# Kernel tuning notes

Hardware: AMD Instinct MI355X
Metric: run time of the kernel (lower is better)

Reference implementation:

```python
import jax, jax.numpy as jnp
import numpy as np

L, I, H = 4, 256, 512          # layers, input_size, hidden_size
SH, LH, GH = 4, 2, 2            # short/long/global heads
NH, HD, FF = SH + LH + GH, H // (SH + LH + GH), 2 * H
S, B = 1024, 8                  # seq (AST nodes), batch
EPS = 1e-5
NEG = -1e9


def _ln(x, g, b):
    m = jnp.mean(x, axis=-1, keepdims=True)
    v = jnp.var(x, axis=-1, keepdims=True)
    return (x - m) * jax.lax.rsqrt(v + EPS) * g + b


def setup_inputs() -> dict:
    key = jax.random.key(0)
    ks = jax.random.split(key, 10)
    w = lambda k, shape: jax.random.normal(k, shape, jnp.float32) * 0.02
    return {
        "nodes": jax.random.normal(ks[0], (S, B, I), jnp.float32),
        "dist": jax.random.randint(ks[1], (B, S, S), 0, 5, jnp.int32),
        "dense_w": w(ks[2], (H, I)), "dense_b": jnp.zeros((H,), jnp.float32),
        "dense_ln_g": jnp.ones((H,), jnp.float32), "dense_ln_b": jnp.zeros((H,), jnp.float32),
        "qkv_w": w(ks[3], (L, 3 * H, H)), "qkv_b": jnp.zeros((L, 3 * H), jnp.float32),
        "out_w": w(ks[4], (L, H, H)), "out_b": jnp.zeros((L, H), jnp.float32),
        "ln1_g": jnp.ones((L, H), jnp.float32), "ln1_b": jnp.zeros((L, H), jnp.float32),
        "ffn_w1": w(ks[5], (L, FF, H)), "ffn_b1": jnp.zeros((L, FF), jnp.float32),
        "ffn_w2": w(ks[6], (L, H, FF)), "ffn_b2": jnp.zeros((L, H), jnp.float32),
        "ln2_g": jnp.ones((L, H), jnp.float32), "ln2_b": jnp.zeros((L, H), jnp.float32),
        "bn_g": jnp.ones((H,), jnp.float32), "bn_b": jnp.zeros((H,), jnp.float32),
    }


def _mask_bias(dist):
    # dist: [B,S,S] int -> additive bias [B,NH,S,S]
    short = (dist == 1)[:, None]                       # [B,1,S,S]
    longm = (dist >= 1)[:, None]
    globm = jnp.broadcast_to((dist[:, 0:1, :] >= 1)[:, None], (dist.shape[0], 1, S, S))
    allowed = jnp.concatenate([
        jnp.broadcast_to(short, (dist.shape[0], SH, S, S)),
        jnp.broadcast_to(longm, (dist.shape[0], LH, S, S)),
        jnp.broadcast_to(globm, (dist.shape[0], GH, S, S)),
    ], axis=1)
    allowed = allowed | jnp.eye(S, dtype=bool)
    return jnp.where(allowed, 0.0, NEG).astype(jnp.float32)


def _forward(nodes, dist, dense_w, dense_b, dense_ln_g, dense_ln_b,
             qkv_w, qkv_b, out_w, out_b, ln1_g, ln1_b,
             ffn_w1, ffn_b1, ffn_w2, ffn_b2, ln2_g, ln2_b, bn_g, bn_b):
    x = jnp.transpose(nodes, (1, 0, 2))                # [B,S,I]
    x = _ln(x @ dense_w.T + dense_b, dense_ln_g, dense_ln_b)  # [B,S,H]
    bias = _mask_bias(dist)                            # [B,NH,S,S]
    scale = 1.0 / np.sqrt(HD)

    def layer(x, p):
        (wqkv, bqkv, wo, bo, g1, b1, w1, bf1, w2, bf2, g2, b2) = p
        qkv = x @ wqkv.T + bqkv                        # [B,S,3H]
        q, k, v = jnp.split(qkv, 3, axis=-1)
        q = q.reshape(B, S, NH, HD).transpose(0, 2, 1, 3)
        k = k.reshape(B, S, NH, HD).transpose(0, 2, 1, 3)
        v = v.reshape(B, S, NH, HD).transpose(0, 2, 1, 3)
        scores = jnp.einsum('bhqd,bhkd->bhqk', q, k) * scale + bias
        attn = jax.nn.softmax(scores, axis=-1)
        o = jnp.einsum('bhqk,bhkd->bhqd', attn, v)
        o = o.transpose(0, 2, 1, 3).reshape(B, S, H) @ wo.T + bo
        x = _ln(x + o, g1, b1)
        f = jax.nn.relu(x @ w1.T + bf1) @ w2.T + bf2
        x = _ln(x + f, g2, b2)
        return x, None

    params = (qkv_w, qkv_b, out_w, out_b, ln1_g, ln1_b,
              ffn_w1, ffn_b1, ffn_w2, ffn_b2, ln2_g, ln2_b)
    x, _ = jax.lax.scan(layer, x, params)
    hidden = x[:, 0]                                   # first token -> [B,H]
    m = jnp.mean(hidden, axis=0)
    v = jnp.var(hidden, axis=0)
    return (hidden - m) * jax.lax.rsqrt(v + EPS) * bn_g + bn_b


def reference(nodes, dist, dense_w, dense_b, dense_ln_g, dense_ln_b,
              qkv_w, qkv_b, out_w, out_b, ln1_g, ln1_b,
              ffn_w1, ffn_b1, ffn_w2, ffn_b2, ln2_g, ln2_b, bn_g, bn_b):
    return _forward(nodes, dist, dense_w, dense_b, dense_ln_g, dense_ln_b,
                    qkv_w, qkv_b, out_w, out_b, ln1_g, ln1_b,
                    ffn_w1, ffn_b1, ffn_w2, ffn_b2, ln2_g, ln2_b, bn_g, bn_b)
```

## Files before the change

### kernel.cpp

```cpp
#include <hip/hip_runtime.h>
#include <hip/hip_bf16.h>
#include <math.h>

#define LAYERS 4
#define IDIM 256
#define HDIM 512
#define NH 8
#define HD 64
#define FF 1024
#define SEQ 1024
#define BATCH 8
#define EPS 1e-5f

typedef __attribute__((ext_vector_type(8))) short short8;
typedef __attribute__((ext_vector_type(4))) short short4v;
typedef __attribute__((ext_vector_type(4))) float f32x4;
typedef __attribute__((ext_vector_type(4))) int int4v;
typedef __attribute__((ext_vector_type(4))) unsigned int uint4v;
typedef unsigned long long u64;

__device__ __forceinline__ short f2bf(float f) {
    unsigned u = __float_as_uint(f);
    u = (u + 0x7FFFu + ((u >> 16) & 1u)) >> 16;
    return (short)u;
}
__device__ __forceinline__ float bf2f(short s) {
    return __uint_as_float(((unsigned)(unsigned short)s) << 16);
}
__device__ __forceinline__ void gll16(const void* g, void* l) {
    __builtin_amdgcn_global_load_lds(
        (const __attribute__((address_space(1))) unsigned int*)g,
        (__attribute__((address_space(3))) unsigned int*)l, 16, 0, 0);
}
__device__ __forceinline__ float fexp2(float x) {
#if __has_builtin(__builtin_amdgcn_exp2f)
    return __builtin_amdgcn_exp2f(x);
#else
    return exp2f(x);
#endif
}

#define CVT_P0 131072u
#define CVT_P1 3276800u
#define CVT_P2 4325376u
#define CVT_P3 6422528u
#define CVT_TOT 8519680u
#define PREP_W 8320
#define PREP_N 2048
__global__ __launch_bounds__(256) void prep_all(
    const float* __restrict__ s0, short* __restrict__ d0,
    const float* __restrict__ s1, short* __restrict__ d1,
    const float* __restrict__ s2, short* __restrict__ d2,
    const float* __restrict__ s3, short* __restrict__ d3,
    const float* __restrict__ s4, short* __restrict__ d4,
    const float* __restrict__ nodes, short* __restrict__ xt,
    const int* __restrict__ dist, u64* __restrict__ mS,
    u64* __restrict__ mL, u64* __restrict__ mG) {
    int blk = blockIdx.x;
    if (blk < PREP_W) {
        size_t i = ((size_t)blk * 256 + threadIdx.x) * 4;
        const float* s; short* d; size_t off;
        if (i < CVT_P0)      { s = s0; d = d0; off = i; }
        else if (i < CVT_P1) { s = s1; d = d1; off = i - CVT_P0; }
        else if (i < CVT_P2) { s = s2; d = d2; off = i - CVT_P1; }
        else if (i < CVT_P3) { s = s3; d = d3; off = i - CVT_P2; }
        else                 { s = s4; d = d4; off = i - CVT_P3; }
        f32x4 f = *(const f32x4*)(s + off);
        short4v o = {f2bf(f[0]), f2bf(f[1]), f2bf(f[2]), f2bf(f[3])};
        *(short4v*)(d + off) = o;
    } else if (blk < PREP_W + PREP_N) {
        size_t idx = ((size_t)(blk - PREP_W) * 256 + threadIdx.x) * 4;
        int i  = idx & (IDIM - 1);
        int sb = idx >> 8;
        int b  = sb & (BATCH - 1);
        int s  = sb >> 3;
        f32x4 f = *(const f32x4*)(nodes + idx);
        short4v o = {f2bf(f[0]), f2bf(f[1]), f2bf(f[2]), f2bf(f[3])};
        *(short4v*)(xt + ((size_t)b * SEQ + s) * IDIM + i) = o;
    } else {
        int blk2 = blk - (PREP_W + PREP_N);
        int b = blk2 >> 10, q = blk2 & 1023;
        int wv = threadIdx.x >> 6, lane = threadIdx.x & 63;
        const int* dp = dist + ((size_t)b * SEQ + q) * SEQ;
        size_t mbase = ((size_t)b * SEQ + q) * 16;
#pragma unroll
        for (int it = 0; it < 4; it++) {
            int w64 = it * 4 + wv;
            int d = dp[w64 * 64 + lane];
            u64 bs = __ballot(d == 1);
            u64 bl = __ballot(d >= 1);
            if (lane == 0) {
                mS[mbase + w64] = bs;
                mL[mbase + w64] = bl;
                if (q == 0) mG[b * 16 + w64] = bl;
            }
        }
    }
}

template<int BM, int BK>
__global__ __launch_bounds__(256, 2)
void gemm_bf16(const short* __restrict__ A, const short* __restrict__ W,
               const float* __restrict__ bias, short* __restrict__ C,
               short* __restrict__ vt, int M, int N, int K, int relu) {
    constexpr int UPR = BK / 8;
    constexpr int RPC = 512 / BK;
    __shared__ __align__(16) short As[BM * BK];
    __shared__ __align__(16) short Ws[128 * BK];
    const int tid = threadIdx.x;
    const int w = tid >> 6, lane = tid & 63;
    const int l15 = lane & 15, quad = lane >> 4;
    const int m0 = blockIdx.y * BM, n0 = blockIdx.x * 128;

    constexpr int NI = (BM == 128) ? 4 : 2;
    const int wm = (BM == 128) ? (w >> 1) * 64 : 0;
    const int wn = (BM == 128) ? (w & 1) * 64 : w * 32;

    f32x4 acc[4][NI];
#pragma unroll
    for (int mi = 0; mi < 4; mi++)
#pragma unroll
        for (int ni = 0; ni < NI; ni++) acc[mi][ni] = (f32x4){0.f, 0.f, 0.f, 0.f};

    const int r_in = (BK == 64) ? (lane >> 3) : (lane >> 4);
    const int c8   = lane & (UPR - 1);

    for (int k0 = 0; k0 < K; k0 += BK) {
#pragma unroll
        for (int rep = 0; rep < BM * BK / 2048; rep++) {
            int chunk = rep * 4 + w;
            int row = chunk * RPC + r_in;
            const short* src = A + (size_t)(m0 + row) * K + k0 + ((c8 ^ (row & (UPR - 1))) << 3);
            gll16(src, (char*)As + chunk * 1024);
        }
#pragma unroll
        for (int rep = 0; rep < 128 * BK / 2048; rep++) {
            int chunk = rep * 4 + w;
            int row = chunk * RPC + r_in;
            const short* src = W + (size_t)(n0 + row) * K + k0 + ((c8 ^ (row & (UPR - 1))) << 3);
            gll16(src, (char*)Ws + chunk * 1024);
        }
        __syncthreads();
#pragma unroll
        for (int ks = 0; ks < BK / 32; ks++) {
            short8 af[4], wf[NI];
            const int dblk = ks * 4 + quad;
#pragma unroll
            for (int mi = 0; mi < 4; mi++) {
                int row = wm + mi * 16 + l15;
                af[mi] = *(const short8*)((const char*)As + row * (BK * 2) + ((dblk ^ (row & (UPR - 1))) << 4));
            }
#pragma unroll
            for (int ni = 0; ni < NI; ni++) {
                int row = wn + ni * 16 + l15;
                wf[ni] = *(const short8*)((const char*)Ws + row * (BK * 2) + ((dblk ^ (row & (UPR - 1))) << 4));
            }
#pragma unroll
            for (int mi = 0; mi < 4; mi++)
#pragma unroll
                for (int ni = 0; ni < NI; ni++)
                    acc[mi][ni] = __builtin_amdgcn_mfma_f32_16x16x32_bf16(
                        af[mi], wf[ni], acc[mi][ni], 0, 0, 0);
        }
        __syncthreads();
    }
    if (vt && n0 >= 1024) {
#pragma unroll
        for (int ni = 0; ni < NI; ni++) {
            int n = n0 + wn + ni * 16 + l15;
            int d = n - 1024, h = d >> 6, dd = d & 63;
            float bz = bias[n];
#pragma unroll
            for (int mi = 0; mi < 4; mi++) {
                int mbase = m0 + wm + mi * 16 + quad * 4;
                int b = mbase >> 10, s = mbase & 1023;
                size_t off = ((size_t)(b * NH + h) * HD + dd) * SEQ + s;
                short4v pk;
#pragma unroll
                for (int r = 0; r < 4; r++) pk[r] = f2bf(acc[mi][ni][r] + bz);
                *(short4v*)(vt + off) = pk;
            }
        }
    } else {
#pragma unroll
        for (int ni = 0; ni < NI; ni++) {
            int n = n0 + wn + ni * 16 + l15;
            float bz = bias[n];
#pragma unroll
            for (int mi = 0; mi < 4; mi++) {
#pragma unroll
                for (int r = 0; r < 4; r++) {
                    int m = m0 + wm + mi * 16 + quad * 4 + r;
                    float v = acc[mi][ni][r] + bz;
                    if (relu) v = fmaxf(v, 0.f);
                    C[(size_t)m * N + n] = f2bf(v);
                }
            }
        }
    }
}

#define EXP2SC 0.18033688011112042f
__global__ __launch_bounds__(256, 4)
void attn_mfma(const short* __restrict__ qkv, const short* __restrict__ vt,
               const u64* __restrict__ maskS, const u64* __restrict__ maskL,
               const u64* __restrict__ maskG, short* __restrict__ out) {
    const int tid = threadIdx.x;
    const int w = tid >> 6, lane = tid & 63, l15 = lane & 15, quad = lane >> 4;
    const int p = blockIdx.x;
    const int g_ = (p & 7) + 8 * (p >> 7);
    const int qt = (p >> 3) & 15;
    const int b = g_ >> 3, h = g_ & 7;
    const int q = qt * 64 + w * 16 + l15;

    __shared__ __align__(16) short Ks[128 * 64];
    __shared__ __align__(16) short Vs[128 * 64];

    short8 qf[2];
    {
        const short* qrow = qkv + ((size_t)(b * SEQ + q) * 1536) + h * 64;
#pragma unroll
        for (int ks = 0; ks < 2; ks++)
            qf[ks] = *(const short8*)(qrow + ks * 32 + quad * 8);
    }
    const u64* mrow = (h < 4) ? (maskS + ((size_t)b * SEQ + q) * 16)
                   : (h < 6) ? (maskL + ((size_t)b * SEQ + q) * 16)
                   :           (maskG + (size_t)b * 16);

    f32x4 of[4];
#pragma unroll
    for (int mt = 0; mt < 4; mt++) of[mt] = (f32x4){0.f, 0.f, 0.f, 0.f};
    float ls0 = 0.f, ls1 = 0.f;

    const int r_in = lane >> 3, c8 = lane & 7;
    const int swz = (c8 ^ r_in) << 3;
    const short* kbase = qkv + ((size_t)b * SEQ) * 1536 + 512 + h * 64 + swz;
    const short* vp = vt + ((size_t)((b * NH + h) * HD) + r_in) * SEQ + swz;
    const int fsw = (l15 & 7);

    for (int kt = 0; kt < SEQ; kt += 128) {
#pragma unroll
        for (int rep = 0; rep < 4; rep++) {
            int c = rep * 4 + w;
            int pr = c * 8 + r_in;
            int pt = pr & 63;
            int key = (pr & 64) | (pt & 32) | (((pt >> 2) & 3) << 3)
                    | (((pt >> 4) & 1) << 2) | (pt & 3);
            gll16(kbase + (size_t)(kt + key) * 1536, (char*)Ks + c * 1024);
        }
#pragma unroll
        for (int rep = 0; rep < 4; rep++) {
            int v = rep * 4 + w;
            gll16(vp + (size_t)((v & 7) * 8) * SEQ + kt + (v >> 3) * 64,
                  (char*)Vs + v * 1024);
        }
        __syncthreads();

#pragma unroll
        for (int t = 0; t < 2; t++) {
            f32x4 sa[4];
#pragma unroll
            for (int g = 0; g < 4; g++) sa[g] = (f32x4){0.f, 0.f, 0.f, 0.f};
#pragma unroll
            for (int ks = 0; ks < 2; ks++) {
                const int dblk = ks * 4 + quad;
#pragma unroll
                for (int g = 0; g < 4; g++) {
                    int row = t * 64 + g * 16 + l15;
                    short8 kf = *(const short8*)((const char*)Ks + row * 128 + ((dblk ^ fsw) << 4));
                    sa[g] = __builtin_amdgcn_mfma_f32_16x16x32_bf16(kf, qf[ks], sa[g], 0, 0, 0);
                }
            }
            u64 mw = mrow[(kt >> 6) + t];
            if ((q >> 6) == (kt >> 6) + t) mw |= 1ull << (q & 63);
            u64 mq2 = mw >> (quad * 8);
            unsigned mlo = (unsigned)mq2, mhi = (unsigned)(mq2 >> 32);
            float pv[4][4];
#pragma unroll
            for (int g = 0; g < 4; g++) {
                unsigned mg = ((g & 2) ? mhi : mlo) >> ((g & 1) * 4);
#pragma unroll
                for (int r = 0; r < 4; r++) {
                    float e = fexp2(sa[g][r] * EXP2SC);
                    e = ((mg >> r) & 1u) ? e : 0.f;
                    pv[g][r] = e;
                    if (g & 1) ls1 += e; else ls0 += e;
                }
            }
            short8 pfrag[2];
#pragma unroll
            for (int g32 = 0; g32 < 2; g32++) {
                uint4v pk;
                pk[0] = __builtin_amdgcn_perm(__float_as_uint(pv[2 * g32][1]),
                                              __float_as_uint(pv[2 * g32][0]), 0x07060302u);
                pk[1] = __builtin_amdgcn_perm(__float_as_uint(pv[2 * g32][3]),
                                              __float_as_uint(pv[2 * g32][2]), 0x07060302u);
                pk[2] = __builtin_amdgcn_perm(__float_as_uint(pv[2 * g32 + 1][1]),
                                              __float_as_uint(pv[2 * g32 + 1][0]), 0x07060302u);
                pk[3] = __builtin_amdgcn_perm(__float_as_uint(pv[2 * g32 + 1][3]),
                                              __float_as_uint(pv[2 * g32 + 1][2]), 0x07060302u);
                pfrag[g32] = __builtin_bit_cast(short8, pk);
            }
#pragma unroll
            for (int g32 = 0; g32 < 2; g32++) {
                const int u = g32 * 4 + quad;
#pragma unroll
                for (int mt = 0; mt < 4; mt++) {
                    int row = mt * 16 + l15;
                    short8 vf = *(const short8*)((const char*)Vs + t * 8192 + row * 128 + ((u ^ fsw) << 4));
                    of[mt] = __builtin_amdgcn_mfma_f32_16x16x32_bf16(vf, pfrag[g32], of[mt], 0, 0, 0);
                }
            }
        }
        __syncthreads();
    }
    float lsum = ls0 + ls1;
    lsum += __shfl_xor(lsum, 16);
    lsum += __shfl_xor(lsum, 32);
    float inv = 1.f / lsum;
#pragma unroll
    for (int mt = 0; mt < 4; mt++) {
        short4v pk;
#pragma unroll
        for (int r = 0; r < 4; r++) pk[r] = f2bf(of[mt][r] * inv);
        *(short4v*)(out + ((size_t)(b * SEQ + q) * HDIM) + h * 64 + mt * 16 + quad * 4) = pk;
    }
}

__global__ __launch_bounds__(256) void ln_bf16(const short* __restrict__ x,
                                               const short* __restrict__ r,
                                               const float* __restrict__ g,
                                               const float* __restrict__ b,
                                               short* __restrict__ y) {
    const int wv = threadIdx.x >> 6, lane = threadIdx.x & 63;
    const size_t row = (size_t)blockIdx.x * 4 + wv;
    const size_t base = row * HDIM + lane * 8;
    short8 xv = *(const short8*)(x + base);
    float v[8];
#pragma unroll
    for (int i = 0; i < 8; i++) v[i] = bf2f(xv[i]);
    if (r) {
        short8 rv = *(const short8*)(r + base);
#pragma unroll
        for (int i = 0; i < 8; i++) v[i] += bf2f(rv[i]);
    }
    float s = 0.f, ss = 0.f;
#pragma unroll
    for (int i = 0; i < 8; i++) { s += v[i]; ss += v[i] * v[i]; }
#pragma unroll
    for (int off = 1; off < 64; off <<= 1) {
        s  += __shfl_xor(s, off);
        ss += __shfl_xor(ss, off);
    }
    const float mean = s * (1.f / HDIM);
    const float var  = ss * (1.f / HDIM) - mean * mean;
    const float inv  = rsqrtf(var + EPS);
    f32x4 g0 = *(const f32x4*)(g + lane * 8), g1 = *(const f32x4*)(g + lane * 8 + 4);
    f32x4 b0 = *(const f32x4*)(b + lane * 8), b1 = *(const f32x4*)(b + lane * 8 + 4);
    short8 o;
#pragma unroll
    for (int i = 0; i < 4; i++) o[i]     = f2bf((v[i]     - mean) * inv * g0[i] + b0[i]);
#pragma unroll
    for (int i = 0; i < 4; i++) o[i + 4] = f2bf((v[i + 4] - mean) * inv * g1[i] + b1[i]);
    *(short8*)(y + base) = o;
}

__global__ __launch_bounds__(256) void final_bn(const short* __restrict__ X,
                                                const float* __restrict__ g,
                                                const float* __restrict__ bb,
                                                float* __restrict__ out) {
    int h = blockIdx.x * 256 + threadIdx.x;
    if (h >= HDIM) return;
    float vals[BATCH];
    float m = 0.f;
#pragma unroll
    for (int b = 0; b < BATCH; b++) {
        vals[b] = bf2f(X[(size_t)b * SEQ * HDIM + h]);
        m += vals[b];
    }
    m *= (1.f / BATCH);
    float v = 0.f;
#pragma unroll
    for (int b = 0; b < BATCH; b++) { float d = vals[b] - m; v += d * d; }
    v *= (1.f / BATCH);
    float inv = rsqrtf(v + EPS);
#pragma unroll
    for (int b = 0; b < BATCH; b++)
        out[b * HDIM + h] = (vals[b] - m) * inv * g[h] + bb[h];
}

extern "C" void kernel_launch(void* const* d_in, const int* in_sizes, int n_in,
                              void* d_out, int out_size, void* d_ws, size_t ws_size,
                              hipStream_t stream) {
    const float* nodes      = (const float*)d_in[0];
    const int*   dist       = (const int*)  d_in[1];
    const float* dense_w    = (const float*)d_in[2];
    const float* dense_b    = (const float*)d_in[3];
    const float* dense_ln_g = (const float*)d_in[4];
    const float* dense_ln_b = (const float*)d_in[5];
    const float* qkv_w      = (const float*)d_in[6];
    const float* qkv_b      = (const float*)d_in[7];
    const float* out_w      = (const float*)d_in[8];
    const float* out_b      = (const float*)d_in[9];
    const float* ln1_g      = (const float*)d_in[10];
    const float* ln1_b      = (const float*)d_in[11];
    const float* ffn_w1     = (const float*)d_in[12];
    const float* ffn_b1     = (const float*)d_in[13];
    const float* ffn_w2     = (const float*)d_in[14];
    const float* ffn_b2     = (const float*)d_in[15];
    const float* ln2_g      = (const float*)d_in[16];
    const float* ln2_b      = (const float*)d_in[17];
    const float* bn_g       = (const float*)d_in[18];
    const float* bn_b       = (const float*)d_in[19];
    float* out = (float*)d_out;

    const int M = BATCH * SEQ;
    const size_t MB = 1024 * 1024;
    char* ws = (char*)d_ws;
    short* Wd   = (short*)(ws + 0 * MB);
    short* Wqkv = (short*)(ws + 1 * MB);
    short* Wo   = (short*)(ws + 9 * MB);
    short* W1   = (short*)(ws + 13 * MB);
    short* W2   = (short*)(ws + 18 * MB);
    u64*   mS   = (u64*)(ws + 23 * MB);
    u64*   mL   = (u64*)(ws + 24 * MB);
    u64*   mG   = (u64*)(ws + 25 * MB);
    short* X    = (short*)(ws + 26 * MB);
    short* QKV  = (short*)(ws + 34 * MB);
    short* Vt   = (short*)(ws + 58 * MB);
    short* AT   = (short*)(ws + 66 * MB);
    short* O2   = (short*)(ws + 74 * MB);
    short* XT   = QKV;
    short* F1   = QKV;
    short* F2   = AT;

    prep_all<<<PREP_W + PREP_N + BATCH * SEQ, 256, 0, stream>>>(
        dense_w, Wd, qkv_w, Wqkv, out_w, Wo, ffn_w1, W1, ffn_w2, W2,
        nodes, XT, dist, mS, mL, mG);

    gemm_bf16<64, 128><<<dim3(HDIM / 128, M / 64), 256, 0, stream>>>(
        XT, Wd, dense_b, O2, nullptr, M, HDIM, IDIM, 0);
    ln_bf16<<<M / 4, 256, 0, stream>>>(O2, nullptr, dense_ln_g, dense_ln_b, X);

    for (int l = 0; l < LAYERS; l++) {
        const short* wqkv = Wqkv + (size_t)l * 3 * HDIM * HDIM;
        const float* bqkv = qkv_b + (size_t)l * 3 * HDIM;
        const short* wo   = Wo + (size_t)l * HDIM * HDIM;
        const float* bo   = out_b + (size_t)l * HDIM;
        const short* w1   = W1 + (size_t)l * FF * HDIM;
        const float* b1   = ffn_b1 + (size_t)l * FF;
        const short* w2   = W2 + (size_t)l * HDIM * FF;
        const float* b2   = ffn_b2 + (size_t)l * HDIM;

        gemm_bf16<128, 64><<<dim3(3 * HDIM / 128, M / 128), 256, 0, stream>>>(
            X, wqkv, bqkv, QKV, Vt, M, 3 * HDIM, HDIM, 0);
        attn_mfma<<<1024, 256, 0, stream>>>(QKV, Vt, mS, mL, mG, AT);
        gemm_bf16<64, 128><<<dim3(HDIM / 128, M / 64), 256, 0, stream>>>(
            AT, wo, bo, O2, nullptr, M, HDIM, HDIM, 0);
        ln_bf16<<<M / 4, 256, 0, stream>>>(X, O2, ln1_g + l * HDIM, ln1_b + l * HDIM, X);
        gemm_bf16<128, 64><<<dim3(FF / 128, M / 128), 256, 0, stream>>>(
            X, w1, b1, F1, nullptr, M, FF, HDIM, 1);
        gemm_bf16<64, 128><<<dim3(HDIM / 128, M / 64), 256, 0, stream>>>(
            F1, w2, b2, F2, nullptr, M, HDIM, FF, 0);
        ln_bf16<<<M / 4, 256, 0, stream>>>(X, F2, ln2_g + l * HDIM, ln2_b + l * HDIM, X);
    }
    final_bn<<<(HDIM + 255) / 256, 256, 0, stream>>>(X, bn_g, bn_b, out);
}
```

Measured before the change: 613.5 us.

## Fuse output-projection GEMMs with residual add and LayerNorm in one kernel

Adds a gemm_ln kernel in which each 512-thread block computes a full 32-row by 512-column output tile, then applies bias, the residual add and LayerNorm in registers with a cross-wave reduction through shared memory. It replaces the dense, attention-output and FFN2 GEMMs plus their separate ln_bf16 launches, removing the intermediate round trip through global memory and nine kernel launches. The cost is a 32-row M tile that reloads the whole 512-row weight slice per block, giving only 256 blocks at one block per CU, plus a residual read in place alongside the X write, which is safe only because each block touches just its own rows.

```diff
diff --git a/kernel.cpp b/kernel.cpp
--- a/kernel.cpp
+++ b/kernel.cpp
@@ -200,6 +200,135 @@
     }
 }
 
+template<int K, bool RES>
+__global__ __launch_bounds__(512, 1)
+void gemm_ln(const short* __restrict__ A, const short* __restrict__ W,
+             const float* __restrict__ bias, const short* __restrict__ resid,
+             const float* __restrict__ g, const float* __restrict__ bta,
+             short* __restrict__ Y) {
+    constexpr int BK = 64, BM = 32, NW = 512, NT = K / BK;
+    __shared__ __align__(16) short As[2][BM * BK];
+    __shared__ __align__(16) short Ws[2][NW * BK];
+    const int tid = threadIdx.x, w = tid >> 6, lane = tid & 63;
+    const int l15 = lane & 15, quad = lane >> 4;
+    const int m0 = blockIdx.x * BM;
+    const int r_in = lane >> 3, c8 = lane & 7;
+    const int swz = (c8 ^ r_in) << 3;
+
+    f32x4 acc[2][4];
+#pragma unroll
+    for (int mi = 0; mi < 2; mi++)
+#pragma unroll
+        for (int ni = 0; ni < 4; ni++) acc[mi][ni] = (f32x4){0.f, 0.f, 0.f, 0.f};
+
+#define STAGE_LN(bf, k0)                                                          \
+    do {                                                                          \
+        if (w < 4) {                                                              \
+            int row_ = w * 8 + r_in;                                              \
+            gll16(A + (size_t)(m0 + row_) * K + (k0) + swz,                       \
+                  (char*)As[bf] + w * 1024);                                      \
+        }                                                                         \
+        _Pragma("unroll")                                                         \
+        for (int rep_ = 0; rep_ < 8; rep_++) {                                    \
+            int chunk_ = rep_ * 8 + w;                                            \
+            int row_ = chunk_ * 8 + r_in;                                         \
+            gll16(W + (size_t)row_ * K + (k0) + swz,                              \
+                  (char*)Ws[bf] + chunk_ * 1024);                                 \
+        }                                                                         \
+    } while (0)
+
+    STAGE_LN(0, 0);
+    __syncthreads();
+    int cur = 0;
+    for (int t = 0; t < NT; t++) {
+        if (t + 1 < NT) STAGE_LN(cur ^ 1, (t + 1) * BK);
+#pragma unroll
+        for (int ks = 0; ks < 2; ks++) {
+            const int dblk = ks * 4 + quad;
+            short8 af[2];
+#pragma unroll
+            for (int mi = 0; mi < 2; mi++) {
+                int row = mi * 16 + l15;
+                af[mi] = *(const short8*)((const char*)As[cur] + row * 128 + ((dblk ^ (row & 7)) << 4));
+            }
+#pragma unroll
+            for (int ni = 0; ni < 4; ni++) {
+                int row = w * 64 + ni * 16 + l15;
+                short8 wf = *(const short8*)((const char*)Ws[cur] + row * 128 + ((dblk ^ (row & 7)) << 4));
+#pragma unroll
+                for (int mi = 0; mi < 2; mi++)
+                    acc[mi][ni] = __builtin_amdgcn_mfma_f32_16x16x32_bf16(
+                        wf, af[mi], acc[mi][ni], 0, 0, 0);
+            }
+        }
+        __syncthreads();
+        cur ^= 1;
+    }
+#undef STAGE_LN
+
+    float sum[2] = {0.f, 0.f}, sq[2] = {0.f, 0.f};
+#pragma unroll
+    for (int mi = 0; mi < 2; mi++)
+#pragma unroll
+        for (int ni = 0; ni < 4; ni++) {
+            int nb = w * 64 + ni * 16 + quad * 4;
+            f32x4 bz = *(const f32x4*)(bias + nb);
+            f32x4 v;
+            if (RES) {
+                short4v rv = *(const short4v*)(resid + (size_t)(m0 + mi * 16 + l15) * NW + nb);
+#pragma unroll
+                for (int r = 0; r < 4; r++) v[r] = acc[mi][ni][r] + bz[r] + bf2f(rv[r]);
+            } else {
+#pragma unroll
+                for (int r = 0; r < 4; r++) v[r] = acc[mi][ni][r] + bz[r];
+            }
+            acc[mi][ni] = v;
+            sum[mi] += v[0] + v[1] + v[2] + v[3];
+            sq[mi]  += v[0] * v[0] + v[1] * v[1] + v[2] * v[2] + v[3] * v[3];
+        }
+#pragma unroll
+    for (int mi = 0; mi < 2; mi++) {
+        sum[mi] += __shfl_xor(sum[mi], 16); sum[mi] += __shfl_xor(sum[mi], 32);
+        sq[mi]  += __shfl_xor(sq[mi], 16);  sq[mi]  += __shfl_xor(sq[mi], 32);
+    }
+    float* red = (float*)As;
+    if (quad == 0) {
+#pragma unroll
+        for (int mi = 0; mi < 2; mi++) {
+            red[(mi * 16 + l15) * 8 + w]       = sum[mi];
+            red[256 + (mi * 16 + l15) * 8 + w] = sq[mi];
+        }
+    }
+    __syncthreads();
+    float mean[2], inv[2];
+#pragma unroll
+    for (int mi = 0; mi < 2; mi++) {
+        f32x4 s0 = *(const f32x4*)(red + (mi * 16 + l15) * 8);
+        f32x4 s1 = *(const f32x4*)(red + (mi * 16 + l15) * 8 + 4);
+        f32x4 q0 = *(const f32x4*)(red + 256 + (mi * 16 + l15) * 8);
+        f32x4 q1 = *(const f32x4*)(red + 256 + (mi * 16 + l15) * 8 + 4);
+        float st = s0[0] + s0[1] + s0[2] + s0[3] + s1[0] + s1[1] + s1[2] + s1[3];
+        float qt = q0[0] + q0[1] + q0[2] + q0[3] + q1[0] + q1[1] + q1[2] + q1[3];
+        float mn = st * (1.f / NW);
+        float vr = qt * (1.f / NW) - mn * mn;
+        mean[mi] = mn;
+        inv[mi]  = rsqrtf(vr + EPS);
+    }
+#pragma unroll
+    for (int mi = 0; mi < 2; mi++)
+#pragma unroll
+        for (int ni = 0; ni < 4; ni++) {
+            int nb = w * 64 + ni * 16 + quad * 4;
+            f32x4 gv = *(const f32x4*)(g + nb);
+            f32x4 bv = *(const f32x4*)(bta + nb);
+            short4v pk;
+#pragma unroll
+            for (int r = 0; r < 4; r++)
+                pk[r] = f2bf((acc[mi][ni][r] - mean[mi]) * inv[mi] * gv[r] + bv[r]);
+            *(short4v*)(Y + (size_t)(m0 + mi * 16 + l15) * NW + nb) = pk;
+        }
+}
+
 #define EXP2SC 0.18033688011112042f
 __global__ __launch_bounds__(256, 4)
 void attn_mfma(const short* __restrict__ qkv, const short* __restrict__ vt,
@@ -325,44 +454,6 @@
         for (int r = 0; r < 4; r++) pk[r] = f2bf(of[mt][r] * inv);
         *(short4v*)(out + ((size_t)(b * SEQ + q) * HDIM) + h * 64 + mt * 16 + quad * 4) = pk;
     }
-}
-
-__global__ __launch_bounds__(256) void ln_bf16(const short* __restrict__ x,
-                                               const short* __restrict__ r,
-                                               const float* __restrict__ g,
-                                               const float* __restrict__ b,
-                                               short* __restrict__ y) {
-    const int wv = threadIdx.x >> 6, lane = threadIdx.x & 63;
-    const size_t row = (size_t)blockIdx.x * 4 + wv;
-    const size_t base = row * HDIM + lane * 8;
-    short8 xv = *(const short8*)(x + base);
-    float v[8];
-#pragma unroll
-    for (int i = 0; i < 8; i++) v[i] = bf2f(xv[i]);
-    if (r) {
-        short8 rv = *(const short8*)(r + base);
-#pragma unroll
-        for (int i = 0; i < 8; i++) v[i] += bf2f(rv[i]);
-    }
-    float s = 0.f, ss = 0.f;
-#pragma unroll
-    for (int i = 0; i < 8; i++) { s += v[i]; ss += v[i] * v[i]; }
-#pragma unroll
-    for (int off = 1; off < 64; off <<= 1) {
-        s  += __shfl_xor(s, off);
-        ss += __shfl_xor(ss, off);
-    }
-    const float mean = s * (1.f / HDIM);
-    const float var  = ss * (1.f / HDIM) - mean * mean;
-    const float inv  = rsqrtf(var + EPS);
-    f32x4 g0 = *(const f32x4*)(g + lane * 8), g1 = *(const f32x4*)(g + lane * 8 + 4);
-    f32x4 b0 = *(const f32x4*)(b + lane * 8), b1 = *(const f32x4*)(b + lane * 8 + 4);
-    short8 o;
-#pragma unroll
-    for (int i = 0; i < 4; i++) o[i]     = f2bf((v[i]     - mean) * inv * g0[i] + b0[i]);
-#pragma unroll
-    for (int i = 0; i < 4; i++) o[i + 4] = f2bf((v[i + 4] - mean) * inv * g1[i] + b1[i]);
-    *(short8*)(y + base) = o;
 }
 
 __global__ __launch_bounds__(256) void final_bn(const short* __restrict__ X,
@@ -429,18 +520,15 @@
     short* QKV  = (short*)(ws + 34 * MB);
     short* Vt   = (short*)(ws + 58 * MB);
     short* AT   = (short*)(ws + 66 * MB);
-    short* O2   = (short*)(ws + 74 * MB);
     short* XT   = QKV;
     short* F1   = QKV;
-    short* F2   = AT;
 
     prep_all<<<PREP_W + PREP_N + BATCH * SEQ, 256, 0, stream>>>(
         dense_w, Wd, qkv_w, Wqkv, out_w, Wo, ffn_w1, W1, ffn_w2, W2,
         nodes, XT, dist, mS, mL, mG);
 
-    gemm_bf16<64, 128><<<dim3(HDIM / 128, M / 64), 256, 0, stream>>>(
-        XT, Wd, dense_b, O2, nullptr, M, HDIM, IDIM, 0);
-    ln_bf16<<<M / 4, 256, 0, stream>>>(O2, nullptr, dense_ln_g, dense_ln_b, X);
+    gemm_ln<IDIM, false><<<M / 32, 512, 0, stream>>>(
+        XT, Wd, dense_b, nullptr, dense_ln_g, dense_ln_b, X);
 
     for (int l = 0; l < LAYERS; l++) {
         const short* wqkv = Wqkv + (size_t)l * 3 * HDIM * HDIM;
@@ -455,14 +543,12 @@
         gemm_bf16<128, 64><<<dim3(3 * HDIM / 128, M / 128), 256, 0, stream>>>(
             X, wqkv, bqkv, QKV, Vt, M, 3 * HDIM, HDIM, 0);
         attn_mfma<<<1024, 256, 0, stream>>>(QKV, Vt, mS, mL, mG, AT);
-        gemm_bf16<64, 128><<<dim3(HDIM / 128, M / 64), 256, 0, stream>>>(
-            AT, wo, bo, O2, nullptr, M, HDIM, HDIM, 0);
-        ln_bf16<<<M / 4, 256, 0, stream>>>(X, O2, ln1_g + l * HDIM, ln1_b + l * HDIM, X);
+        gemm_ln<HDIM, true><<<M / 32, 512, 0, stream>>>(
+            AT, wo, bo, X, ln1_g + l * HDIM, ln1_b + l * HDIM, X);
         gemm_bf16<128, 64><<<dim3(FF / 128, M / 128), 256, 0, stream>>>(
             X, w1, b1, F1, nullptr, M, FF, HDIM, 1);
-        gemm_bf16<64, 128><<<dim3(HDIM / 128, M / 64), 256, 0, stream>>>(
-            F1, w2, b2, F2, nullptr, M, HDIM, FF, 0);
-        ln_bf16<<<M / 4, 256, 0, stream>>>(X, F2, ln2_g + l * HDIM, ln2_b + l * HDIM, X);
+        gemm_ln<FF, true><<<M / 32, 512, 0, stream>>>(
+            F1, w2, b2, X, ln2_g + l * HDIM, ln2_b + l * HDIM, X);
     }
     final_bn<<<(HDIM + 255) / 256, 256, 0, stream>>>(X, bn_g, bn_b, out);
 }
```

Measured after the change: 622.7 us. Within noise of the previous version (+1.5%).
